# Kernel tuning notes

Measured on AMD Instinct MI355X. Metric: run time of the kernel, lower is better.

## Reference

```python
import jax, jax.numpy as jnp
import numpy as np

HEAD_NUM, HEAD_DIM, HIDDEN = 16, 64, 1024


def setup_inputs() -> dict:
    key = jax.random.key(0)
    ks = jax.random.split(key, 9)
    s = 1.0 / np.sqrt(HIDDEN)
    x = jax.random.normal(ks[0], (4, 2048, HIDDEN), dtype=jnp.float32)
    Wq = jax.random.uniform(ks[1], (HIDDEN, HIDDEN), jnp.float32, -s, s)
    bq = jax.random.uniform(ks[2], (HIDDEN,), jnp.float32, -s, s)
    Wk = jax.random.uniform(ks[3], (HIDDEN, HIDDEN), jnp.float32, -s, s)
    bk = jax.random.uniform(ks[4], (HIDDEN,), jnp.float32, -s, s)
    Wv = jax.random.uniform(ks[5], (HIDDEN, HIDDEN), jnp.float32, -s, s)
    bv = jax.random.uniform(ks[6], (HIDDEN,), jnp.float32, -s, s)
    Wo = jax.random.uniform(ks[7], (HIDDEN, HIDDEN), jnp.float32, -s, s)
    bo = jax.random.uniform(ks[8], (HIDDEN,), jnp.float32, -s, s)
    return {"x": x, "Wq": Wq, "bq": bq, "Wk": Wk, "bk": bk,
            "Wv": Wv, "bv": bv, "Wo": Wo, "bo": bo}


def reference(x, Wq, bq, Wk, bk, Wv, bv, Wo, bo):
    B, S, _ = x.shape
    H, D = HEAD_NUM, HEAD_DIM
    # Linear: x @ W^T + b (torch nn.Linear convention)
    q = (x @ Wq.T + bq).reshape(B, S, H, D).transpose(0, 2, 1, 3)  # [B,H,S,D]
    k = (x @ Wk.T + bk).reshape(B, S, H, D).transpose(0, 2, 1, 3)
    v = (x @ Wv.T + bv).reshape(B, S, H, D).transpose(0, 2, 1, 3)
    scores = jnp.einsum('bhqd,bhkd->bhqk', q, k) / np.sqrt(D)  # [B,H,S,S]
    attn = jax.nn.softmax(scores, axis=-1)  # dropout p=0.0 -> identity
    out = jnp.einsum('bhqk,bhkd->bhqd', attn, v)
    out = out.transpose(0, 2, 1, 3).reshape(B, S, H * D)
    return out @ Wo.T + bo
```

## Files before the change

### kernel.cpp

```cpp
#include <hip/hip_runtime.h>
#include <hip/hip_bf16.h>


typedef __attribute__((ext_vector_type(8))) short short8;
typedef __attribute__((ext_vector_type(4))) short short4b;
typedef __attribute__((ext_vector_type(4))) float floatx4;

#define HID 1024
#define SEQ 2048
#define BATCH 4
#define NH 16
#define HD 64
#define M_TOT (BATCH * SEQ)

#define BM 128
#define BN 128
#define BK 64

#define SCALE2 0.1803368801111204f

typedef const __attribute__((address_space(1))) void g_void;
typedef __attribute__((address_space(3))) void lds_void;

static __device__ __forceinline__ ushort f2bf(float f) {
    union { float f; unsigned int u; } v;
    v.f = f;
    unsigned int u = v.u;
    return (ushort)((u + 0x7fffu + ((u >> 16) & 1u)) >> 16);
}
static __device__ __forceinline__ ushort4 f4tobf(float4 f) {
    ushort4 r;
    r.x = f2bf(f.x); r.y = f2bf(f.y); r.z = f2bf(f.z); r.w = f2bf(f.w);
    return r;
}
static __device__ __forceinline__ unsigned int fbits(float f) {
    union { float f; unsigned int u; } v; v.f = f; return v.u;
}

#define X_F4 (M_TOT * HID / 4)
#define W_F4 (HID * HID / 4)

__global__ __launch_bounds__(256) void convert_bf16(
    const float* __restrict__ x,
    const float* __restrict__ wq, const float* __restrict__ wk,
    const float* __restrict__ wv, const float* __restrict__ wo,
    ushort* __restrict__ xo,
    ushort* __restrict__ wqo, ushort* __restrict__ wko,
    ushort* __restrict__ wvo, ushort* __restrict__ woo)
{
    long i = (long)blockIdx.x * 256 + threadIdx.x;
    const float4* src; ushort4* dst; long off;
    if (i < X_F4)                  { src = (const float4*)x;  dst = (ushort4*)xo;  off = i; }
    else if (i < X_F4 + W_F4)      { src = (const float4*)wq; dst = (ushort4*)wqo; off = i - X_F4; }
    else if (i < X_F4 + 2 * W_F4)  { src = (const float4*)wk; dst = (ushort4*)wko; off = i - X_F4 - W_F4; }
    else if (i < X_F4 + 3 * W_F4)  { src = (const float4*)wv; dst = (ushort4*)wvo; off = i - X_F4 - 2 * W_F4; }
    else                           { src = (const float4*)wo; dst = (ushort4*)woo; off = i - X_F4 - 3 * W_F4; }
    dst[off] = f4tobf(src[off]);
}

template <int MODE>
__global__ __launch_bounds__(256) void gemm_bf(
    const ushort* __restrict__ A,
    const ushort* __restrict__ W0, const ushort* __restrict__ W1,
    const ushort* __restrict__ W2,
    const float* __restrict__ b0, const float* __restrict__ b1,
    const float* __restrict__ b2,
    ushort* __restrict__ o0, ushort* __restrict__ o1, ushort* __restrict__ o2,
    float* __restrict__ of)
{
    __shared__ ushort As[BM * BK];
    __shared__ ushort Bs[BN * BK];

    const int tid  = threadIdx.x;
    const int wave = tid >> 6;
    const int lane = tid & 63;
    const int l16  = lane & 15;
    const int lq   = lane >> 4;

    const int m0 = blockIdx.x * BM;
    const int n0 = blockIdx.y * BN;
    const int z  = (MODE == 1) ? blockIdx.z : 0;

    const ushort* W   = (z == 0) ? W0 : (z == 1) ? W1 : W2;
    const float* bias = (z == 0) ? b0 : (z == 1) ? b1 : b2;

    const int wm = (wave & 1) * 64;
    const int wn = (wave >> 1) * 64;

    const int srow = lane >> 3;
    const int schk = (lane & 7) ^ srow;
    const ushort* gA = A + (size_t)(m0 + wave * 32 + srow) * HID + schk * 8;
    const ushort* gW = W + (size_t)(n0 + wave * 32 + srow) * HID + schk * 8;
    ushort* lA = As + (wave * 32) * BK;
    ushort* lB = Bs + (wave * 32) * BK;

    floatx4 acc[4][4];
#pragma unroll
    for (int i = 0; i < 4; i++)
#pragma unroll
        for (int j = 0; j < 4; j++)
            acc[i][j] = (floatx4){0.f, 0.f, 0.f, 0.f};

    for (int k0 = 0; k0 < HID; k0 += BK) {
        __syncthreads();
#pragma unroll
        for (int i = 0; i < 4; i++) {
            __builtin_amdgcn_global_load_lds(
                (g_void*)(gA + (size_t)(8 * i) * HID + k0),
                (lds_void*)(lA + (8 * i) * BK), 16, 0, 0);
            __builtin_amdgcn_global_load_lds(
                (g_void*)(gW + (size_t)(8 * i) * HID + k0),
                (lds_void*)(lB + (8 * i) * BK), 16, 0, 0);
        }
        __syncthreads();

        const int sw = l16 & 7;
#pragma unroll
        for (int kk8 = 0; kk8 < 8; kk8 += 4) {
            short8 a[4], b[4];
#pragma unroll
            for (int i = 0; i < 4; i++)
                a[i] = *(const short8*)(&As[(wm + i * 16 + l16) * BK + ((lq + kk8) ^ sw) * 8]);
#pragma unroll
            for (int j = 0; j < 4; j++)
                b[j] = *(const short8*)(&Bs[(wn + j * 16 + l16) * BK + ((lq + kk8) ^ sw) * 8]);
#pragma unroll
            for (int i = 0; i < 4; i++)
#pragma unroll
                for (int j = 0; j < 4; j++)
                    acc[i][j] = __builtin_amdgcn_mfma_f32_16x16x32_bf16(
                        a[i], b[j], acc[i][j], 0, 0, 0);
        }
    }

    if (MODE == 0) {
#pragma unroll
        for (int j = 0; j < 4; j++) {
            int n = n0 + wn + j * 16 + l16;
            float bv = bias[n];
#pragma unroll
            for (int i = 0; i < 4; i++)
#pragma unroll
                for (int r = 0; r < 4; r++) {
                    int m = m0 + wm + i * 16 + lq * 4 + r;
                    of[(size_t)m * HID + n] = acc[i][j][r] + bv;
                }
        }
    } else if (z == 2) {
        ushort* out = o2;
#pragma unroll
        for (int j = 0; j < 4; j++) {
            int n = n0 + wn + j * 16 + l16;
            float bv = bias[n];
            int h_ = n >> 6, d_ = n & (HD - 1);
#pragma unroll
            for (int i = 0; i < 4; i++) {
                int m = m0 + wm + i * 16 + lq * 4;
                int b_ = m >> 11, s0 = m & (SEQ - 1);
                ushort4 pk;
                pk.x = f2bf(acc[i][j][0] + bv);
                pk.y = f2bf(acc[i][j][1] + bv);
                pk.z = f2bf(acc[i][j][2] + bv);
                pk.w = f2bf(acc[i][j][3] + bv);
                *(ushort4*)(out + (((size_t)b_ * NH + h_) * HD + d_) * SEQ + s0) = pk;
            }
        }
    } else {
        ushort* out = (z == 0) ? o0 : o1;
        const float sc = (z == 0) ? SCALE2 : 1.0f;
#pragma unroll
        for (int j = 0; j < 4; j++) {
            int n = n0 + wn + j * 16 + l16;
            float bv = bias[n];
            int h_ = n >> 6, d_ = n & (HD - 1);
#pragma unroll
            for (int i = 0; i < 4; i++)
#pragma unroll
                for (int r = 0; r < 4; r++) {
                    int m = m0 + wm + i * 16 + lq * 4 + r;
                    int b_ = m >> 11, s_ = m & (SEQ - 1);
                    out[(((size_t)b_ * NH + h_) * SEQ + s_) * HD + d_] =
                        f2bf((acc[i][j][r] + bv) * sc);
                }
        }
    }
}

__global__ __launch_bounds__(256) void attn_flash(
    const ushort* __restrict__ q, const ushort* __restrict__ k,
    const ushort* __restrict__ v, ushort* __restrict__ o)
{
    __shared__ ushort Ks[64 * 64];
    __shared__ ushort Vs[64 * 64];

    const int tid  = threadIdx.x;
    const int wave = tid >> 6;
    const int lane = tid & 63;
    const int l16  = lane & 15;
    const int lq   = lane >> 4;
    const int e    = l16 & 7;

    const int qb = blockIdx.x;
    const int bh = blockIdx.y;
    const int b_ = bh >> 4, h_ = bh & 15;

    const size_t base = (size_t)bh * SEQ * HD;
    const ushort* Q  = q + base;
    const ushort* K  = k + base;
    const ushort* Vt = v + base;

    const int q0 = qb * 64 + wave * 16;

    short8 qf[2];
    {
        const ushort* qrow = Q + (size_t)(q0 + l16) * HD;
        qf[0] = *(const short8*)(qrow + lq * 8);
        qf[1] = *(const short8*)(qrow + 32 + lq * 8);
    }

    const int srow = lane >> 3;
    const int schk = (lane & 7) ^ srow;
    const ushort* gK = K  + (size_t)(wave * 8 + srow) * HD  + schk * 8;
    const ushort* gV = Vt + (size_t)(wave * 8 + srow) * SEQ + schk * 8;

    floatx4 oacc[4];
#pragma unroll
    for (int jd = 0; jd < 4; jd++) oacc[jd] = (floatx4){0.f, 0.f, 0.f, 0.f};
    float l_ = 0.f;

    const int c0 = lq ^ e;
    const int c1 = (lq + 4) ^ e;

    for (int t = 0; t < SEQ / 64; t++) {
        __syncthreads();
#pragma unroll
        for (int i = 0; i < 2; i++) {
            __builtin_amdgcn_global_load_lds(
                (g_void*)(gK + (size_t)(t * 64 + i * 32) * HD),
                (lds_void*)(Ks + (i * 32 + wave * 8) * 64), 16, 0, 0);
            __builtin_amdgcn_global_load_lds(
                (g_void*)(gV + (size_t)(i * 32) * SEQ + t * 64),
                (lds_void*)(Vs + (i * 32 + wave * 8) * 64), 16, 0, 0);
        }
        __syncthreads();

        floatx4 st[4];
#pragma unroll
        for (int j = 0; j < 4; j++) {
            short8 kf0 = *(const short8*)(&Ks[(j * 16 + l16) * 64 + c0 * 8]);
            short8 kf1 = *(const short8*)(&Ks[(j * 16 + l16) * 64 + c1 * 8]);
            floatx4 zz = (floatx4){0.f, 0.f, 0.f, 0.f};
            zz = __builtin_amdgcn_mfma_f32_16x16x32_bf16(kf0, qf[0], zz, 0, 0, 0);
            st[j] = __builtin_amdgcn_mfma_f32_16x16x32_bf16(kf1, qf[1], zz, 0, 0, 0);
        }

        short4b pf[4];
        float rs = 0.f;
#pragma unroll
        for (int j = 0; j < 4; j++) {
            float p0 = __builtin_amdgcn_exp2f(st[j][0]);
            float p1 = __builtin_amdgcn_exp2f(st[j][1]);
            float p2 = __builtin_amdgcn_exp2f(st[j][2]);
            float p3 = __builtin_amdgcn_exp2f(st[j][3]);
            rs += (p0 + p1) + (p2 + p3);
            union { unsigned int u[2]; short4b s; } pk;
            pk.u[0] = __builtin_amdgcn_perm(fbits(p1), fbits(p0), 0x07060302u);
            pk.u[1] = __builtin_amdgcn_perm(fbits(p3), fbits(p2), 0x07060302u);
            pf[j] = pk.s;
        }
        l_ += rs;

#pragma unroll
        for (int j = 0; j < 4; j++) {
#pragma unroll
            for (int jd = 0; jd < 4; jd++) {
                short4b vf = *(const short4b*)(
                    &Vs[(jd * 16 + l16) * 64 + ((2 * j + (lq >> 1)) ^ e) * 8 + (lq & 1) * 4]);
                oacc[jd] = __builtin_amdgcn_mfma_f32_16x16x16bf16_1k(
                    vf, pf[j], oacc[jd], 0, 0, 0);
            }
        }
    }

    l_ += __shfl_xor(l_, 16, 64);
    l_ += __shfl_xor(l_, 32, 64);

    {
        int qg = q0 + l16;
        float invl = 1.0f / l_;
#pragma unroll
        for (int jd = 0; jd < 4; jd++) {
            ushort4 pk;
            pk.x = f2bf(oacc[jd][0] * invl);
            pk.y = f2bf(oacc[jd][1] * invl);
            pk.z = f2bf(oacc[jd][2] * invl);
            pk.w = f2bf(oacc[jd][3] * invl);
            *(ushort4*)(o + ((size_t)b_ * SEQ + qg) * HID + h_ * HD + jd * 16 + lq * 4) = pk;
        }
    }
}

extern "C" void kernel_launch(void* const* d_in, const int* in_sizes, int n_in,
                              void* d_out, int out_size, void* d_ws, size_t ws_size,
                              hipStream_t stream)
{
    const float* x  = (const float*)d_in[0];
    const float* Wq = (const float*)d_in[1];
    const float* bq = (const float*)d_in[2];
    const float* Wk = (const float*)d_in[3];
    const float* bk = (const float*)d_in[4];
    const float* Wv = (const float*)d_in[5];
    const float* bv = (const float*)d_in[6];
    const float* Wo = (const float*)d_in[7];
    const float* bo = (const float*)d_in[8];
    float* out = (float*)d_out;

    const size_t TE = (size_t)M_TOT * HID;
    const size_t WE = (size_t)HID * HID;
    ushort* qws = (ushort*)d_ws;
    ushort* kws = qws + TE;
    ushort* vws = kws + TE;
    ushort* xbf = vws + TE;
    ushort* aws = xbf;
    ushort* wqb = xbf + TE;
    ushort* wkb = wqb + WE;
    ushort* wvb = wkb + WE;
    ushort* wob = wvb + WE;

    convert_bf16<<<(X_F4 + 4 * W_F4) / 256, 256, 0, stream>>>(
        x, Wq, Wk, Wv, Wo, xbf, wqb, wkb, wvb, wob);

    dim3 g1(M_TOT / BM, HID / BN, 3);
    gemm_bf<1><<<g1, 256, 0, stream>>>(xbf, wqb, wkb, wvb, bq, bk, bv,
                                       qws, kws, vws, nullptr);

    dim3 g2(SEQ / 64, BATCH * NH, 1);
    attn_flash<<<g2, 256, 0, stream>>>(qws, kws, vws, aws);

    dim3 g3(M_TOT / BM, HID / BN, 1);
    gemm_bf<0><<<g3, 256, 0, stream>>>(aws, wob, wob, wob, bo, bo, bo,
                                       nullptr, nullptr, nullptr, out);
}
```

Before: 331.1 us.

## Double-buffer K/V tiles in flash attention and store Q transposed

The attention kernel now keeps two LDS buffers for K and V. It prefetches the next tile with global_load_lds while computing on the current one, which cuts the syncs per iteration from two to one. The QKV projection now writes Q in the transposed [d, seq] layout with packed 4-wide stores, the same as V. The attention kernel reads Q with strided scalar loads to match. Launch bounds gain an occupancy hint of 4. LDS use doubles, which may limit occupancy, and the one-time Q load becomes uncoalesced.

```diff
diff --git a/kernel.cpp b/kernel.cpp
--- a/kernel.cpp
+++ b/kernel.cpp
@@ -146,8 +146,26 @@
                     of[(size_t)m * HID + n] = acc[i][j][r] + bv;
                 }
         }
-    } else if (z == 2) {
-        ushort* out = o2;
+    } else if (z == 1) {
+        ushort* out = o1;
+#pragma unroll
+        for (int j = 0; j < 4; j++) {
+            int n = n0 + wn + j * 16 + l16;
+            float bv = bias[n];
+            int h_ = n >> 6, d_ = n & (HD - 1);
+#pragma unroll
+            for (int i = 0; i < 4; i++)
+#pragma unroll
+                for (int r = 0; r < 4; r++) {
+                    int m = m0 + wm + i * 16 + lq * 4 + r;
+                    int b_ = m >> 11, s_ = m & (SEQ - 1);
+                    out[(((size_t)b_ * NH + h_) * SEQ + s_) * HD + d_] =
+                        f2bf(acc[i][j][r] + bv);
+                }
+        }
+    } else {
+        ushort* out = (z == 0) ? o0 : o2;
+        const float sc = (z == 0) ? SCALE2 : 1.0f;
 #pragma unroll
         for (int j = 0; j < 4; j++) {
             int n = n0 + wn + j * 16 + l16;
@@ -158,40 +176,22 @@
                 int m = m0 + wm + i * 16 + lq * 4;
                 int b_ = m >> 11, s0 = m & (SEQ - 1);
                 ushort4 pk;
-                pk.x = f2bf(acc[i][j][0] + bv);
-                pk.y = f2bf(acc[i][j][1] + bv);
-                pk.z = f2bf(acc[i][j][2] + bv);
-                pk.w = f2bf(acc[i][j][3] + bv);
+                pk.x = f2bf((acc[i][j][0] + bv) * sc);
+                pk.y = f2bf((acc[i][j][1] + bv) * sc);
+                pk.z = f2bf((acc[i][j][2] + bv) * sc);
+                pk.w = f2bf((acc[i][j][3] + bv) * sc);
                 *(ushort4*)(out + (((size_t)b_ * NH + h_) * HD + d_) * SEQ + s0) = pk;
             }
         }
-    } else {
-        ushort* out = (z == 0) ? o0 : o1;
-        const float sc = (z == 0) ? SCALE2 : 1.0f;
-#pragma unroll
-        for (int j = 0; j < 4; j++) {
-            int n = n0 + wn + j * 16 + l16;
-            float bv = bias[n];
-            int h_ = n >> 6, d_ = n & (HD - 1);
-#pragma unroll
-            for (int i = 0; i < 4; i++)
-#pragma unroll
-                for (int r = 0; r < 4; r++) {
-                    int m = m0 + wm + i * 16 + lq * 4 + r;
-                    int b_ = m >> 11, s_ = m & (SEQ - 1);
-                    out[(((size_t)b_ * NH + h_) * SEQ + s_) * HD + d_] =
-                        f2bf((acc[i][j][r] + bv) * sc);
-                }
-        }
-    }
-}
-
-__global__ __launch_bounds__(256) void attn_flash(
+    }
+}
+
+__global__ __launch_bounds__(256, 4) void attn_flash(
     const ushort* __restrict__ q, const ushort* __restrict__ k,
     const ushort* __restrict__ v, ushort* __restrict__ o)
 {
-    __shared__ ushort Ks[64 * 64];
-    __shared__ ushort Vs[64 * 64];
+    __shared__ ushort Ks[2 * 64 * 64];
+    __shared__ ushort Vs[2 * 64 * 64];
 
     const int tid  = threadIdx.x;
     const int wave = tid >> 6;
@@ -205,17 +205,17 @@
     const int b_ = bh >> 4, h_ = bh & 15;
 
     const size_t base = (size_t)bh * SEQ * HD;
-    const ushort* Q  = q + base;
+    const ushort* Qt = q + base;
     const ushort* K  = k + base;
     const ushort* Vt = v + base;
 
     const int q0 = qb * 64 + wave * 16;
 
     short8 qf[2];
-    {
-        const ushort* qrow = Q + (size_t)(q0 + l16) * HD;
-        qf[0] = *(const short8*)(qrow + lq * 8);
-        qf[1] = *(const short8*)(qrow + 32 + lq * 8);
+#pragma unroll
+    for (int jj = 0; jj < 8; jj++) {
+        qf[0][jj] = (short)Qt[(size_t)(lq * 8 + jj) * SEQ + q0 + l16];
+        qf[1][jj] = (short)Qt[(size_t)(32 + lq * 8 + jj) * SEQ + q0 + l16];
     }
 
     const int srow = lane >> 3;
@@ -231,24 +231,40 @@
     const int c0 = lq ^ e;
     const int c1 = (lq + 4) ^ e;
 
+#pragma unroll
+    for (int i = 0; i < 2; i++) {
+        __builtin_amdgcn_global_load_lds(
+            (g_void*)(gK + (size_t)(i * 32) * HD),
+            (lds_void*)(Ks + (i * 32 + wave * 8) * 64), 16, 0, 0);
+        __builtin_amdgcn_global_load_lds(
+            (g_void*)(gV + (size_t)(i * 32) * SEQ),
+            (lds_void*)(Vs + (i * 32 + wave * 8) * 64), 16, 0, 0);
+    }
+
     for (int t = 0; t < SEQ / 64; t++) {
         __syncthreads();
-#pragma unroll
-        for (int i = 0; i < 2; i++) {
-            __builtin_amdgcn_global_load_lds(
-                (g_void*)(gK + (size_t)(t * 64 + i * 32) * HD),
-                (lds_void*)(Ks + (i * 32 + wave * 8) * 64), 16, 0, 0);
-            __builtin_amdgcn_global_load_lds(
-                (g_void*)(gV + (size_t)(i * 32) * SEQ + t * 64),
-                (lds_void*)(Vs + (i * 32 + wave * 8) * 64), 16, 0, 0);
-        }
-        __syncthreads();
+
+        if (t + 1 < SEQ / 64) {
+            const int nb = (t + 1) & 1;
+#pragma unroll
+            for (int i = 0; i < 2; i++) {
+                __builtin_amdgcn_global_load_lds(
+                    (g_void*)(gK + (size_t)((t + 1) * 64 + i * 32) * HD),
+                    (lds_void*)(Ks + nb * 4096 + (i * 32 + wave * 8) * 64), 16, 0, 0);
+                __builtin_amdgcn_global_load_lds(
+                    (g_void*)(gV + (size_t)(i * 32) * SEQ + (t + 1) * 64),
+                    (lds_void*)(Vs + nb * 4096 + (i * 32 + wave * 8) * 64), 16, 0, 0);
+            }
+        }
+
+        const ushort* Kb = Ks + (t & 1) * 4096;
+        const ushort* Vb = Vs + (t & 1) * 4096;
 
         floatx4 st[4];
 #pragma unroll
         for (int j = 0; j < 4; j++) {
-            short8 kf0 = *(const short8*)(&Ks[(j * 16 + l16) * 64 + c0 * 8]);
-            short8 kf1 = *(const short8*)(&Ks[(j * 16 + l16) * 64 + c1 * 8]);
+            short8 kf0 = *(const short8*)(&Kb[(j * 16 + l16) * 64 + c0 * 8]);
+            short8 kf1 = *(const short8*)(&Kb[(j * 16 + l16) * 64 + c1 * 8]);
             floatx4 zz = (floatx4){0.f, 0.f, 0.f, 0.f};
             zz = __builtin_amdgcn_mfma_f32_16x16x32_bf16(kf0, qf[0], zz, 0, 0, 0);
             st[j] = __builtin_amdgcn_mfma_f32_16x16x32_bf16(kf1, qf[1], zz, 0, 0, 0);
@@ -275,7 +291,7 @@
 #pragma unroll
             for (int jd = 0; jd < 4; jd++) {
                 short4b vf = *(const short4b*)(
-                    &Vs[(jd * 16 + l16) * 64 + ((2 * j + (lq >> 1)) ^ e) * 8 + (lq & 1) * 4]);
+                    &Vb[(jd * 16 + l16) * 64 + ((2 * j + (lq >> 1)) ^ e) * 8 + (lq & 1) * 4]);
                 oacc[jd] = __builtin_amdgcn_mfma_f32_16x16x16bf16_1k(
                     vf, pf[j], oacc[jd], 0, 0, 0);
             }
```

Measured after the change: 284.5 us. 1.16x faster.
